# Kernel optimization log

Hardware: AMD Instinct MI355X
Metric: run time of the kernel (lower is better)

Reference implementation:

```python
import math
import jax, jax.numpy as jnp
import numpy as np

HIDDEN = 1024
INTER = 2048
NUM_EXPERTS = 8          # includes 1 noop slot (last column)
TOP_K = 2
CAPACITY_FACTOR = 1.0
BATCH, SEQ = 4, 4096


def setup_inputs() -> dict:
    key = jax.random.key(0)
    k_x, k_rw, k_ei, k_eo = jax.random.split(key, 4)
    x = jax.random.normal(k_x, (BATCH, SEQ, HIDDEN), dtype=jnp.float32)
    # Router: nn.Linear(hidden, num_experts) with xavier_uniform weight, zero-ish bias
    limit = math.sqrt(6.0 / (HIDDEN + NUM_EXPERTS))
    router_w = jax.random.uniform(k_rw, (NUM_EXPERTS, HIDDEN), dtype=jnp.float32,
                                  minval=-limit, maxval=limit)
    router_b = jnp.zeros((NUM_EXPERTS,), dtype=jnp.float32)
    # Expert params initialized with randn, exactly as in the torch module
    experts_inter = jax.random.normal(k_ei, (NUM_EXPERTS - 1, HIDDEN, INTER), dtype=jnp.float32)
    experts_out = jax.random.normal(k_eo, (NUM_EXPERTS - 1, INTER, HIDDEN), dtype=jnp.float32)
    return {"x": x, "router_w": router_w, "router_b": router_b,
            "experts_inter": experts_inter, "experts_out": experts_out}


def reference(x, router_w, router_b, experts_inter, experts_out):
    B, S, H = x.shape
    E = router_w.shape[0]
    N = B * S
    capacity = math.ceil(N / E * CAPACITY_FACTOR)  # static (shapes are static)

    x_flat = x.reshape(N, H)
    # Router: linear + softmax over experts
    weights = jax.nn.softmax(x_flat @ router_w.T + router_b, axis=-1)   # [N, E]

    # Top-k sparsification: keep top-k weights per token, zero the rest
    vals, idx = jax.lax.top_k(weights, TOP_K)                            # [N, k]
    topk_w = jnp.zeros_like(weights).at[jnp.arange(N)[:, None], idx].set(vals)

    # Last expert column is the no-op (identity) path
    noop_routed = x_flat * topk_w[:, -1:]                                # [N, H]

    expert_w = topk_w[:, :-1]                                            # [N, E-1]
    mask = (expert_w > 0).astype(jnp.int32)                              # [N, E-1]

    # Per-expert: sort tokens by routing mask (descending), take first `capacity`
    sorted_idx = jnp.argsort(-mask, axis=0)[:capacity]                   # [C, E-1], stable
    sorted_mask = jnp.take_along_axis(mask, sorted_idx, axis=0)          # [C, E-1]

    used_idx = (sorted_idx * sorted_mask).reshape(-1)                    # [C*(E-1)]
    toks = x_flat[used_idx] * sorted_mask.reshape(-1)[:, None].astype(x.dtype)
    toks = toks.reshape(capacity, E - 1, H)                              # [C, E-1, H]
    in_w = jnp.take_along_axis(expert_w, sorted_idx, axis=0)             # [C, E-1]

    # Grouped expert FFN: relu(x W1) W2, weighted by routing prob
    h = jax.nn.relu(jnp.einsum('ceh,ehi->cei', toks, experts_inter))     # [C, E-1, I]
    out = jnp.einsum('cei,eih->ceh', h, experts_out) * in_w[..., None]   # [C, E-1, H]

    # Scatter-add combine (masked slots contribute zeros at index 0)
    combined = jnp.zeros_like(x_flat).at[used_idx].add(out.reshape(-1, H))
    combined = combined + noop_routed
    return combined.reshape(B, S, H)
```

## Files before the change

### kernel.cpp

```cpp
#include <hip/hip_runtime.h>
#include <stdint.h>

#define HIDDEN 1024
#define INTER 2048
#define NEXP 8
#define NE 7
#define NTOK 16384
#define CAP 2048
#define BM 64
#define BN 64
#define BK 64
#define GBM 128
#define GBN 128

typedef __attribute__((ext_vector_type(8))) short short8;
typedef __attribute__((ext_vector_type(4))) float f32x4;

__device__ __forceinline__ unsigned short f2bf(float f) {
  union { float f; unsigned int u; } v;
  v.f = f;
  unsigned int u = v.u;
  unsigned int r = (u + 0x7FFFu + ((u >> 16) & 1u)) >> 16;
  return (unsigned short)r;
}

typedef __attribute__((address_space(1))) const unsigned int gu32;
typedef __attribute__((address_space(3))) unsigned int lu32;
__device__ __forceinline__ void gload16(const void* g, void* l) {
  __builtin_amdgcn_global_load_lds((gu32*)g, (lu32*)l, 16, 0, 0);
}

__global__ __launch_bounds__(256) void router_kernel(
    const float* __restrict__ x, const float* __restrict__ rw,
    const float* __restrict__ rb, float* __restrict__ expw,
    float* __restrict__ noopw) {
  int wid = threadIdx.x >> 6;
  int lane = threadIdx.x & 63;
  int token = blockIdx.x * 4 + wid;
  const float* xr = x + (size_t)token * HIDDEN;
  float acc[NEXP];
#pragma unroll
  for (int e = 0; e < NEXP; e++) acc[e] = 0.f;
#pragma unroll
  for (int j = 0; j < HIDDEN / 64; j++) {
    int k = j * 64 + lane;
    float xv = xr[k];
#pragma unroll
    for (int e = 0; e < NEXP; e++) acc[e] = fmaf(xv, rw[e * HIDDEN + k], acc[e]);
  }
#pragma unroll
  for (int e = 0; e < NEXP; e++) {
    float a = acc[e];
#pragma unroll
    for (int off = 32; off > 0; off >>= 1) a += __shfl_xor(a, off);
    acc[e] = a + rb[e];
  }
  if (lane == 0) {
    float m = acc[0];
#pragma unroll
    for (int e = 1; e < NEXP; e++) m = fmaxf(m, acc[e]);
    float w[NEXP];
    float s = 0.f;
#pragma unroll
    for (int e = 0; e < NEXP; e++) { w[e] = expf(acc[e] - m); s += w[e]; }
    float inv = 1.f / s;
#pragma unroll
    for (int e = 0; e < NEXP; e++) w[e] *= inv;
    int t1 = 0;
#pragma unroll
    for (int e = 1; e < NEXP; e++) if (w[e] > w[t1]) t1 = e;
    int t2 = (t1 == 0) ? 1 : 0;
#pragma unroll
    for (int e = 0; e < NEXP; e++) if (e != t1 && w[e] > w[t2]) t2 = e;
    noopw[token] = (t1 == NEXP - 1) ? w[t1] : ((t2 == NEXP - 1) ? w[t2] : 0.f);
#pragma unroll
    for (int e = 0; e < NE; e++) {
      float v = 0.f;
      if (e == t1) v = w[e];
      if (e == t2) v = w[e];
      expw[(size_t)e * NTOK + token] = v;
    }
  }
}

__global__ void assign_kernel(const float* __restrict__ expw,
                              int* __restrict__ slot_tok,
                              float* __restrict__ slot_w) {
  int e = blockIdx.x;
  int lane = threadIdx.x;
  const float* we = expw + (size_t)e * NTOK;
  int base = 0;
  for (int t0 = 0; t0 < NTOK; t0 += 64) {
    float w = we[t0 + lane];
    bool flag = w > 0.f;
    unsigned long long mask = __ballot(flag);
    int prefix = __popcll(mask & ((1ull << lane) - 1ull));
    int pos = base + prefix;
    if (flag && pos < CAP) {
      slot_tok[e * CAP + pos] = t0 + lane;
      slot_w[e * CAP + pos] = w;
    }
    base += __popcll(mask);
    if (base >= CAP) break;
  }
  int cnt = base < CAP ? base : CAP;
  for (int p = cnt + lane; p < CAP; p += 64) {
    slot_tok[e * CAP + p] = -1;
    slot_w[e * CAP + p] = 0.f;
  }
}

__global__ __launch_bounds__(256) void noop_kernel(
    const float* __restrict__ x, const float* __restrict__ noopw,
    float* __restrict__ out) {
  size_t i = (size_t)blockIdx.x * 256 + threadIdx.x;
  float4 v = ((const float4*)x)[i];
  float w = noopw[i >> 8];
  v.x *= w; v.y *= w; v.z *= w; v.w *= w;
  ((float4*)out)[i] = v;
}

__global__ __launch_bounds__(256) void convert_x_kernel(
    const float* __restrict__ x, unsigned short* __restrict__ xbf) {
  size_t i = (size_t)blockIdx.x * 256 + threadIdx.x;
  if (i >= (size_t)(NTOK + 1) * (HIDDEN / 8)) return;
  size_t row = i >> 7;
  short8 p;
  if (row < NTOK) {
    const float* s = x + i * 8;
    float4 v0 = ((const float4*)s)[0];
    float4 v1 = ((const float4*)s)[1];
    p[0] = (short)f2bf(v0.x); p[1] = (short)f2bf(v0.y);
    p[2] = (short)f2bf(v0.z); p[3] = (short)f2bf(v0.w);
    p[4] = (short)f2bf(v1.x); p[5] = (short)f2bf(v1.y);
    p[6] = (short)f2bf(v1.z); p[7] = (short)f2bf(v1.w);
  } else {
    p = (short8){0, 0, 0, 0, 0, 0, 0, 0};
  }
  *(short8*)(xbf + i * 8) = p;
}

__global__ __launch_bounds__(256) void transpose_bf16_kernel(
    const float* __restrict__ in, unsigned short* __restrict__ outp,
    int K, int N) {
  int e = blockIdx.z;
  const float* src = in + (size_t)e * K * N;
  unsigned short* dst = outp + (size_t)e * K * N;
  int k0 = blockIdx.y * 64;
  int n0 = blockIdx.x * 64;
  __shared__ float tile[64][65];
  int tid = threadIdx.x;
  int nr = tid & 15;
  int kr = tid >> 4;
#pragma unroll
  for (int i = 0; i < 4; i++) {
    int k = i * 16 + kr;
    float4 v = *(const float4*)(src + (size_t)(k0 + k) * N + n0 + nr * 4);
    tile[k][nr * 4 + 0] = v.x;
    tile[k][nr * 4 + 1] = v.y;
    tile[k][nr * 4 + 2] = v.z;
    tile[k][nr * 4 + 3] = v.w;
  }
  __syncthreads();
  int g = tid & 7;
  int nb = tid >> 3;
#pragma unroll
  for (int i = 0; i < 2; i++) {
    int n = i * 32 + nb;
    short8 p;
#pragma unroll
    for (int j = 0; j < 8; j++) p[j] = (short)f2bf(tile[g * 8 + j][n]);
    *(short8*)(dst + (size_t)(n0 + n) * K + k0 + g * 8) = p;
  }
}

__global__ __launch_bounds__(256) void gemm1_mfma_kernel(
    const unsigned short* __restrict__ xbf, const unsigned short* __restrict__ wiT,
    const int* __restrict__ slot_tok, unsigned short* __restrict__ h) {
  int e = blockIdx.z;
  const unsigned short* be = wiT + (size_t)e * HIDDEN * INTER;
  unsigned short* he = h + (size_t)e * CAP * INTER;
  int bm0 = blockIdx.y * GBM;
  int bn0 = blockIdx.x * GBN;
  __shared__ __align__(16) unsigned short As[GBM * 64];
  __shared__ __align__(16) unsigned short Bs[GBN * 64];
  int tid = threadIdx.x;
  int lane = tid & 63, w = tid >> 6;
  int wm = w >> 1, wn = w & 1;

  const unsigned short* aptr[4];
  const unsigned short* bptr[4];
#pragma unroll
  for (int c = 0; c < 4; c++) {
    int s = w * 4 + c;
    int r = s * 8 + (lane >> 3);
    int gb = lane & 7;
    int g = gb ^ (r & 7);
    int tok = slot_tok[e * CAP + bm0 + r];
    int row = tok < 0 ? NTOK : tok;
    aptr[c] = xbf + (size_t)row * HIDDEN + g * 8;
    bptr[c] = be + (size_t)(bn0 + r) * HIDDEN + g * 8;
  }

  f32x4 acc[4][4];
#pragma unroll
  for (int i = 0; i < 4; i++)
#pragma unroll
    for (int j = 0; j < 4; j++) acc[i][j] = (f32x4){0.f, 0.f, 0.f, 0.f};

  for (int k0 = 0; k0 < HIDDEN; k0 += 64) {
#pragma unroll
    for (int c = 0; c < 4; c++) gload16(aptr[c] + k0, &As[(w * 4 + c) * 512]);
#pragma unroll
    for (int c = 0; c < 4; c++) gload16(bptr[c] + k0, &Bs[(w * 4 + c) * 512]);
    __syncthreads();
#pragma unroll
    for (int kk = 0; kk < 2; kk++) {
      short8 a[4], b[4];
#pragma unroll
      for (int fm = 0; fm < 4; fm++) {
        int r = wm * 64 + fm * 16 + (lane & 15);
        int gb = (kk * 4 + (lane >> 4)) ^ (r & 7);
        a[fm] = *(const short8*)&As[r * 64 + gb * 8];
      }
#pragma unroll
      for (int fn = 0; fn < 4; fn++) {
        int n = wn * 64 + fn * 16 + (lane & 15);
        int gb = (kk * 4 + (lane >> 4)) ^ (n & 7);
        b[fn] = *(const short8*)&Bs[n * 64 + gb * 8];
      }
#pragma unroll
      for (int fm = 0; fm < 4; fm++)
#pragma unroll
        for (int fn = 0; fn < 4; fn++)
          acc[fm][fn] = __builtin_amdgcn_mfma_f32_16x16x32_bf16(
              a[fm], b[fn], acc[fm][fn], 0, 0, 0);
    }
    __syncthreads();
  }
#pragma unroll
  for (int fm = 0; fm < 4; fm++)
#pragma unroll
    for (int r4 = 0; r4 < 4; r4++) {
      int m = bm0 + wm * 64 + fm * 16 + ((lane >> 4) << 2) + r4;
#pragma unroll
      for (int fn = 0; fn < 4; fn++) {
        int n = bn0 + wn * 64 + fn * 16 + (lane & 15);
        float v = acc[fm][fn][r4];
        he[(size_t)m * INTER + n] = f2bf(v > 0.f ? v : 0.f);
      }
    }
}

__global__ __launch_bounds__(256) void gemm2_mfma_kernel(
    const unsigned short* __restrict__ h, const unsigned short* __restrict__ woT,
    const int* __restrict__ slot_tok, const float* __restrict__ slot_w,
    float* __restrict__ out) {
  int e = blockIdx.z;
  const unsigned short* ae = h + (size_t)e * CAP * INTER;
  const unsigned short* be = woT + (size_t)e * INTER * HIDDEN;
  int bm0 = blockIdx.y * GBM;
  int bn0 = blockIdx.x * GBN;
  __shared__ __align__(16) unsigned short As[GBM * 64];
  __shared__ __align__(16) unsigned short Bs[GBN * 64];
  int tid = threadIdx.x;
  int lane = tid & 63, w = tid >> 6;
  int wm = w >> 1, wn = w & 1;

  const unsigned short* aptr[4];
  const unsigned short* bptr[4];
#pragma unroll
  for (int c = 0; c < 4; c++) {
    int s = w * 4 + c;
    int r = s * 8 + (lane >> 3);
    int gb = lane & 7;
    int g = gb ^ (r & 7);
    aptr[c] = ae + (size_t)(bm0 + r) * INTER + g * 8;
    bptr[c] = be + (size_t)(bn0 + r) * INTER + g * 8;
  }

  f32x4 acc[4][4];
#pragma unroll
  for (int i = 0; i < 4; i++)
#pragma unroll
    for (int j = 0; j < 4; j++) acc[i][j] = (f32x4){0.f, 0.f, 0.f, 0.f};

  for (int k0 = 0; k0 < INTER; k0 += 64) {
#pragma unroll
    for (int c = 0; c < 4; c++) gload16(aptr[c] + k0, &As[(w * 4 + c) * 512]);
#pragma unroll
    for (int c = 0; c < 4; c++) gload16(bptr[c] + k0, &Bs[(w * 4 + c) * 512]);
    __syncthreads();
#pragma unroll
    for (int kk = 0; kk < 2; kk++) {
      short8 a[4], b[4];
#pragma unroll
      for (int fm = 0; fm < 4; fm++) {
        int r = wm * 64 + fm * 16 + (lane & 15);
        int gb = (kk * 4 + (lane >> 4)) ^ (r & 7);
        a[fm] = *(const short8*)&As[r * 64 + gb * 8];
      }
#pragma unroll
      for (int fn = 0; fn < 4; fn++) {
        int n = wn * 64 + fn * 16 + (lane & 15);
        int gb = (kk * 4 + (lane >> 4)) ^ (n & 7);
        b[fn] = *(const short8*)&Bs[n * 64 + gb * 8];
      }
#pragma unroll
      for (int fm = 0; fm < 4; fm++)
#pragma unroll
        for (int fn = 0; fn < 4; fn++)
          acc[fm][fn] = __builtin_amdgcn_mfma_f32_16x16x32_bf16(
              a[fm], b[fn], acc[fm][fn], 0, 0, 0);
    }
    __syncthreads();
  }
#pragma unroll
  for (int fm = 0; fm < 4; fm++)
#pragma unroll
    for (int r4 = 0; r4 < 4; r4++) {
      int m = bm0 + wm * 64 + fm * 16 + ((lane >> 4) << 2) + r4;
      int tok = slot_tok[e * CAP + m];
      float sw = slot_w[e * CAP + m];
      if (tok >= 0) {
#pragma unroll
        for (int fn = 0; fn < 4; fn++) {
          int n = bn0 + wn * 64 + fn * 16 + (lane & 15);
          unsafeAtomicAdd(out + (size_t)tok * HIDDEN + n, acc[fm][fn][r4] * sw);
        }
      }
    }
}

__global__ __launch_bounds__(256) void gemm1_kernel(
    const float* __restrict__ x, const float* __restrict__ wi,
    const int* __restrict__ slot_tok, unsigned short* __restrict__ h,
    int e_base) {
  int e = e_base + blockIdx.z;
  unsigned short* he = h + (size_t)blockIdx.z * ((size_t)CAP * INTER);
  const float* wie = wi + (size_t)e * HIDDEN * INTER;
  int bm0 = blockIdx.y * BM;
  int bn0 = blockIdx.x * BN;
  __shared__ __align__(16) unsigned short As[BM][BK];
  __shared__ __align__(16) unsigned short Bs[BN][BK];
  int tid = threadIdx.x;
  int lane = tid & 63;
  int wid = tid >> 6;
  int wm = wid >> 1, wn = wid & 1;
  int tokA[2];
#pragma unroll
  for (int t = 0; t < 2; t++)
    tokA[t] = slot_tok[e * CAP + bm0 + ((tid + t * 256) >> 3)];
  f32x4 acc[2][2];
#pragma unroll
  for (int i = 0; i < 2; i++)
#pragma unroll
    for (int j = 0; j < 2; j++) acc[i][j] = (f32x4){0.f, 0.f, 0.f, 0.f};
  for (int k0 = 0; k0 < HIDDEN; k0 += BK) {
#pragma unroll
    for (int t = 0; t < 2; t++) {
      int idx = tid + t * 256;
      int r = idx >> 3, g = idx & 7;
      short8 pack;
      if (tokA[t] >= 0) {
        const float* src = x + (size_t)tokA[t] * HIDDEN + k0 + g * 8;
        float4 v0 = ((const float4*)src)[0];
        float4 v1 = ((const float4*)src)[1];
        pack[0] = (short)f2bf(v0.x); pack[1] = (short)f2bf(v0.y);
        pack[2] = (short)f2bf(v0.z); pack[3] = (short)f2bf(v0.w);
        pack[4] = (short)f2bf(v1.x); pack[5] = (short)f2bf(v1.y);
        pack[6] = (short)f2bf(v1.z); pack[7] = (short)f2bf(v1.w);
      } else {
        pack = (short8){0, 0, 0, 0, 0, 0, 0, 0};
      }
      int gs = g ^ (r & 7);
      *(short8*)(&As[r][gs * 8]) = pack;
    }
#pragma unroll
    for (int t = 0; t < 2; t++) {
      int idx = tid + t * 256;
      int k = idx >> 3, g = idx & 7;
      const float* src = wie + (size_t)(k0 + k) * INTER + bn0 + g * 8;
      float4 v0 = ((const float4*)src)[0];
      float4 v1 = ((const float4*)src)[1];
      float f[8] = {v0.x, v0.y, v0.z, v0.w, v1.x, v1.y, v1.z, v1.w};
#pragma unroll
      for (int i2 = 0; i2 < 8; i2++) {
        int n = g * 8 + i2;
        int kc = k ^ ((n & 7) << 3);
        Bs[n][kc] = f2bf(f[i2]);
      }
    }
    __syncthreads();
#pragma unroll
    for (int kk = 0; kk < 2; kk++) {
      short8 a[2], b[2];
#pragma unroll
      for (int fm = 0; fm < 2; fm++) {
        int r = wm * 32 + fm * 16 + (lane & 15);
        int gs = (kk * 4 + (lane >> 4)) ^ (r & 7);
        a[fm] = *(const short8*)(&As[r][gs * 8]);
      }
#pragma unroll
      for (int fn = 0; fn < 2; fn++) {
        int n = wn * 32 + fn * 16 + (lane & 15);
        int gs = (kk * 4 + (lane >> 4)) ^ (n & 7);
        b[fn] = *(const short8*)(&Bs[n][gs * 8]);
      }
#pragma unroll
      for (int fm = 0; fm < 2; fm++)
#pragma unroll
        for (int fn = 0; fn < 2; fn++)
          acc[fm][fn] = __builtin_amdgcn_mfma_f32_16x16x32_bf16(
              a[fm], b[fn], acc[fm][fn], 0, 0, 0);
    }
    __syncthreads();
  }
#pragma unroll
  for (int fm = 0; fm < 2; fm++)
#pragma unroll
    for (int fn = 0; fn < 2; fn++)
#pragma unroll
      for (int r = 0; r < 4; r++) {
        int m = bm0 + wm * 32 + fm * 16 + ((lane >> 4) << 2) + r;
        int n = bn0 + wn * 32 + fn * 16 + (lane & 15);
        float v = acc[fm][fn][r];
        v = v > 0.f ? v : 0.f;
        he[(size_t)m * INTER + n] = f2bf(v);
      }
}

__global__ __launch_bounds__(256) void gemm2_kernel(
    const unsigned short* __restrict__ h, const float* __restrict__ wo,
    const int* __restrict__ slot_tok, const float* __restrict__ slot_w,
    float* __restrict__ out, int e_base) {
  int e = e_base + blockIdx.z;
  const unsigned short* he = h + (size_t)blockIdx.z * ((size_t)CAP * INTER);
  const float* woe = wo + (size_t)e * INTER * HIDDEN;
  int bm0 = blockIdx.y * BM;
  int bn0 = blockIdx.x * BN;
  __shared__ __align__(16) unsigned short As[BM][BK];
  __shared__ __align__(16) unsigned short Bs[BN][BK];
  int tid = threadIdx.x;
  int lane = tid & 63;
  int wid = tid >> 6;
  int wm = wid >> 1, wn = wid & 1;
  f32x4 acc[2][2];
#pragma unroll
  for (int i = 0; i < 2; i++)
#pragma unroll
    for (int j = 0; j < 2; j++) acc[i][j] = (f32x4){0.f, 0.f, 0.f, 0.f};
  for (int k0 = 0; k0 < INTER; k0 += BK) {
#pragma unroll
    for (int t = 0; t < 2; t++) {
      int idx = tid + t * 256;
      int r = idx >> 3, g = idx & 7;
      short8 pack = *(const short8*)(he + (size_t)(bm0 + r) * INTER + k0 + g * 8);
      int gs = g ^ (r & 7);
      *(short8*)(&As[r][gs * 8]) = pack;
    }
#pragma unroll
    for (int t = 0; t < 2; t++) {
      int idx = tid + t * 256;
      int k = idx >> 3, g = idx & 7;
      const float* src = woe + (size_t)(k0 + k) * HIDDEN + bn0 + g * 8;
      float4 v0 = ((const float4*)src)[0];
      float4 v1 = ((const float4*)src)[1];
      float f[8] = {v0.x, v0.y, v0.z, v0.w, v1.x, v1.y, v1.z, v1.w};
#pragma unroll
      for (int i2 = 0; i2 < 8; i2++) {
        int n = g * 8 + i2;
        int kc = k ^ ((n & 7) << 3);
        Bs[n][kc] = f2bf(f[i2]);
      }
    }
    __syncthreads();
#pragma unroll
    for (int kk = 0; kk < 2; kk++) {
      short8 a[2], b[2];
#pragma unroll
      for (int fm = 0; fm < 2; fm++) {
        int r = wm * 32 + fm * 16 + (lane & 15);
        int gs = (kk * 4 + (lane >> 4)) ^ (r & 7);
        a[fm] = *(const short8*)(&As[r][gs * 8]);
      }
#pragma unroll
      for (int fn = 0; fn < 2; fn++) {
        int n = wn * 32 + fn * 16 + (lane & 15);
        int gs = (kk * 4 + (lane >> 4)) ^ (n & 7);
        b[fn] = *(const short8*)(&Bs[n][gs * 8]);
      }
#pragma unroll
      for (int fm = 0; fm < 2; fm++)
#pragma unroll
        for (int fn = 0; fn < 2; fn++)
          acc[fm][fn] = __builtin_amdgcn_mfma_f32_16x16x32_bf16(
              a[fm], b[fn], acc[fm][fn], 0, 0, 0);
    }
    __syncthreads();
  }
#pragma unroll
  for (int fm = 0; fm < 2; fm++)
#pragma unroll
    for (int r = 0; r < 4; r++) {
      int m = bm0 + wm * 32 + fm * 16 + ((lane >> 4) << 2) + r;
      int tok = slot_tok[e * CAP + m];
      float sw = slot_w[e * CAP + m];
      if (tok >= 0) {
#pragma unroll
        for (int fn = 0; fn < 2; fn++) {
          int n = bn0 + wn * 32 + fn * 16 + (lane & 15);
          unsafeAtomicAdd(out + (size_t)tok * HIDDEN + n, acc[fm][fn][r] * sw);
        }
      }
    }
}

extern "C" void kernel_launch(void* const* d_in, const int* in_sizes, int n_in,
                              void* d_out, int out_size, void* d_ws, size_t ws_size,
                              hipStream_t stream) {
  const float* x = (const float*)d_in[0];
  const float* rw = (const float*)d_in[1];
  const float* rb = (const float*)d_in[2];
  const float* wi = (const float*)d_in[3];
  const float* wo = (const float*)d_in[4];
  float* out = (float*)d_out;
  char* ws = (char*)d_ws;

  const size_t h_bytes = (size_t)NE * CAP * INTER * 2;
  const size_t xbf_bytes = (size_t)(NTOK + 1) * HIDDEN * 2;
  const size_t wT_bytes = (size_t)NE * HIDDEN * INTER * 2;
  const size_t P_bytes = xbf_bytes + wT_bytes;
  const size_t small_bytes = (size_t)NE * NTOK * 4 + (size_t)NTOK * 4 +
                             (size_t)NE * CAP * 4 * 2;
  const size_t need_new = h_bytes + P_bytes + small_bytes;

  if (ws_size >= need_new) {
    unsigned short* h = (unsigned short*)ws;
    char* P = ws + h_bytes;
    unsigned short* xbf = (unsigned short*)P;
    unsigned short* wiT = (unsigned short*)(P + xbf_bytes);
    unsigned short* woT = (unsigned short*)P;
    char* smalls = P + P_bytes;
    float* expw = (float*)smalls;
    float* noopw = expw + (size_t)NE * NTOK;
    int* slot_tok = (int*)(noopw + NTOK);
    float* slot_w = (float*)(slot_tok + (size_t)NE * CAP);

    convert_x_kernel<<<((NTOK + 1) * (HIDDEN / 8) + 255) / 256, 256, 0, stream>>>(x, xbf);
    transpose_bf16_kernel<<<dim3(INTER / 64, HIDDEN / 64, NE), 256, 0, stream>>>(
        wi, wiT, HIDDEN, INTER);
    router_kernel<<<NTOK / 4, 256, 0, stream>>>(x, rw, rb, expw, noopw);
    assign_kernel<<<NE, 64, 0, stream>>>(expw, slot_tok, slot_w);
    noop_kernel<<<(NTOK * (HIDDEN / 4)) / 256, 256, 0, stream>>>(x, noopw, out);
    gemm1_mfma_kernel<<<dim3(INTER / GBN, CAP / GBM, NE), 256, 0, stream>>>(
        xbf, wiT, slot_tok, h);
    transpose_bf16_kernel<<<dim3(HIDDEN / 64, INTER / 64, NE), 256, 0, stream>>>(
        wo, woT, INTER, HIDDEN);
    gemm2_mfma_kernel<<<dim3(HIDDEN / GBN, CAP / GBM, NE), 256, 0, stream>>>(
        h, woT, slot_tok, slot_w, out);
    return;
  }

  const size_t h_full = (size_t)NE * CAP * INTER * 2;
  const size_t h_one = (size_t)CAP * INTER * 2;
  bool full = ws_size >= h_full + small_bytes;
  size_t hb = full ? h_full : h_one;
  unsigned short* h = (unsigned short*)ws;
  float* expw = (float*)(ws + hb);
  float* noopw = expw + (size_t)NE * NTOK;
  int* slot_tok = (int*)(noopw + NTOK);
  float* slot_w = (float*)(slot_tok + (size_t)NE * CAP);

  router_kernel<<<NTOK / 4, 256, 0, stream>>>(x, rw, rb, expw, noopw);
  assign_kernel<<<NE, 64, 0, stream>>>(expw, slot_tok, slot_w);
  noop_kernel<<<(NTOK * (HIDDEN / 4)) / 256, 256, 0, stream>>>(x, noopw, out);
  if (full) {
    gemm1_kernel<<<dim3(INTER / BN, CAP / BM, NE), 256, 0, stream>>>(
        x, wi, slot_tok, h, 0);
    gemm2_kernel<<<dim3(HIDDEN / BN, CAP / BM, NE), 256, 0, stream>>>(
        h, wo, slot_tok, slot_w, out, 0);
  } else {
    for (int e = 0; e < NE; e++) {
      gemm1_kernel<<<dim3(INTER / BN, CAP / BM, 1), 256, 0, stream>>>(
          x, wi, slot_tok, h, e);
      gemm2_kernel<<<dim3(HIDDEN / BN, CAP / BM, 1), 256, 0, stream>>>(
          h, wo, slot_tok, slot_w, out, e);
    }
  }
}
```

Baseline: 487.4 us.

## Fuse router, bf16 convert and noop into one prologue; parallelize assignment; swizzle GEMM blocks

```diff
diff --git a/kernel.cpp b/kernel.cpp
--- a/kernel.cpp
+++ b/kernel.cpp
@@ -28,6 +28,326 @@
 typedef __attribute__((address_space(3))) unsigned int lu32;
 __device__ __forceinline__ void gload16(const void* g, void* l) {
   __builtin_amdgcn_global_load_lds((gu32*)g, (lu32*)l, 16, 0, 0);
+}
+
+__global__ __launch_bounds__(256) void prologue_kernel(
+    const float* __restrict__ x, const float* __restrict__ rw,
+    const float* __restrict__ rb, float* __restrict__ expw,
+    float* __restrict__ noopw, unsigned short* __restrict__ xbf,
+    float* __restrict__ out) {
+  if (blockIdx.x == NTOK / 4) {
+    unsigned int* z = (unsigned int*)(xbf + (size_t)NTOK * HIDDEN);
+    z[threadIdx.x] = 0u;
+    z[threadIdx.x + 256] = 0u;
+    return;
+  }
+  int wid = threadIdx.x >> 6;
+  int lane = threadIdx.x & 63;
+  int token = blockIdx.x * 4 + wid;
+  const float* xr = x + (size_t)token * HIDDEN;
+  float4 xv[4];
+  float acc[NEXP];
+#pragma unroll
+  for (int e = 0; e < NEXP; e++) acc[e] = 0.f;
+#pragma unroll
+  for (int j = 0; j < 4; j++) {
+    xv[j] = *(const float4*)(xr + j * 256 + lane * 4);
+#pragma unroll
+    for (int e = 0; e < NEXP; e++) {
+      float4 wv = *(const float4*)(rw + e * HIDDEN + j * 256 + lane * 4);
+      acc[e] = fmaf(xv[j].x, wv.x, acc[e]);
+      acc[e] = fmaf(xv[j].y, wv.y, acc[e]);
+      acc[e] = fmaf(xv[j].z, wv.z, acc[e]);
+      acc[e] = fmaf(xv[j].w, wv.w, acc[e]);
+    }
+  }
+#pragma unroll
+  for (int e = 0; e < NEXP; e++) {
+    float a = acc[e];
+#pragma unroll
+    for (int off = 32; off > 0; off >>= 1) a += __shfl_xor(a, off);
+    acc[e] = a + rb[e];
+  }
+  float nwv = 0.f;
+  if (lane == 0) {
+    float m = acc[0];
+#pragma unroll
+    for (int e = 1; e < NEXP; e++) m = fmaxf(m, acc[e]);
+    float w[NEXP];
+    float s = 0.f;
+#pragma unroll
+    for (int e = 0; e < NEXP; e++) { w[e] = expf(acc[e] - m); s += w[e]; }
+    float inv = 1.f / s;
+#pragma unroll
+    for (int e = 0; e < NEXP; e++) w[e] *= inv;
+    int t1 = 0;
+#pragma unroll
+    for (int e = 1; e < NEXP; e++) if (w[e] > w[t1]) t1 = e;
+    int t2 = (t1 == 0) ? 1 : 0;
+#pragma unroll
+    for (int e = 0; e < NEXP; e++) if (e != t1 && w[e] > w[t2]) t2 = e;
+    nwv = (t1 == NEXP - 1) ? w[t1] : ((t2 == NEXP - 1) ? w[t2] : 0.f);
+    noopw[token] = nwv;
+#pragma unroll
+    for (int e = 0; e < NE; e++) {
+      float v = 0.f;
+      if (e == t1) v = w[e];
+      if (e == t2) v = w[e];
+      expw[(size_t)e * NTOK + token] = v;
+    }
+  }
+  float nw = __shfl(nwv, 0);
+  float* orow = out + (size_t)token * HIDDEN;
+  unsigned short* brow = xbf + (size_t)token * HIDDEN;
+#pragma unroll
+  for (int j = 0; j < 4; j++) {
+    float4 o = xv[j];
+    o.x *= nw; o.y *= nw; o.z *= nw; o.w *= nw;
+    *(float4*)(orow + j * 256 + lane * 4) = o;
+    ushort4 b;
+    b.x = f2bf(xv[j].x); b.y = f2bf(xv[j].y);
+    b.z = f2bf(xv[j].z); b.w = f2bf(xv[j].w);
+    *(ushort4*)(brow + j * 256 + lane * 4) = b;
+  }
+}
+
+__global__ __launch_bounds__(1024) void assign_par_kernel(
+    const float* __restrict__ expw, int* __restrict__ slot_tok,
+    float* __restrict__ slot_w) {
+  int e = blockIdx.x;
+  int tid = threadIdx.x;
+  int lane = tid & 63, w = tid >> 6;
+  __shared__ int wtot[16];
+  const float* we = expw + (size_t)e * NTOK;
+  int base = 0;
+#pragma unroll 1
+  for (int r = 0; r < NTOK / 1024; r++) {
+    int t = r * 1024 + tid;
+    float wv = we[t];
+    bool flag = wv > 0.f;
+    unsigned long long mask = __ballot(flag);
+    int lp = __popcll(mask & ((1ull << lane) - 1ull));
+    if (lane == 0) wtot[w] = __popcll(mask);
+    __syncthreads();
+    int pre = 0, tot = 0;
+#pragma unroll
+    for (int i = 0; i < 16; i++) {
+      int v = wtot[i];
+      pre += (i < w) ? v : 0;
+      tot += v;
+    }
+    int pos = base + pre + lp;
+    if (flag && pos < CAP) {
+      slot_tok[e * CAP + pos] = t;
+      slot_w[e * CAP + pos] = wv;
+    }
+    base += tot;
+    __syncthreads();
+    if (base >= CAP) break;
+  }
+  int cnt = base < CAP ? base : CAP;
+  for (int p = cnt + tid; p < CAP; p += 1024) {
+    slot_tok[e * CAP + p] = -1;
+    slot_w[e * CAP + p] = 0.f;
+  }
+}
+
+__global__ __launch_bounds__(256) void transpose_bf16_kernel(
+    const float* __restrict__ in, unsigned short* __restrict__ outp,
+    int K, int N) {
+  int e = blockIdx.z;
+  const float* src = in + (size_t)e * K * N;
+  unsigned short* dst = outp + (size_t)e * K * N;
+  int k0 = blockIdx.y * 64;
+  int n0 = blockIdx.x * 64;
+  __shared__ float tile[64][65];
+  int tid = threadIdx.x;
+  int nr = tid & 15;
+  int kr = tid >> 4;
+#pragma unroll
+  for (int i = 0; i < 4; i++) {
+    int k = i * 16 + kr;
+    float4 v = *(const float4*)(src + (size_t)(k0 + k) * N + n0 + nr * 4);
+    tile[k][nr * 4 + 0] = v.x;
+    tile[k][nr * 4 + 1] = v.y;
+    tile[k][nr * 4 + 2] = v.z;
+    tile[k][nr * 4 + 3] = v.w;
+  }
+  __syncthreads();
+  int g = tid & 7;
+  int nb = tid >> 3;
+#pragma unroll
+  for (int i = 0; i < 2; i++) {
+    int n = i * 32 + nb;
+    short8 p;
+#pragma unroll
+    for (int j = 0; j < 8; j++) p[j] = (short)f2bf(tile[g * 8 + j][n]);
+    *(short8*)(dst + (size_t)(n0 + n) * K + k0 + g * 8) = p;
+  }
+}
+
+__global__ __launch_bounds__(256) void gemm1_mfma_kernel(
+    const unsigned short* __restrict__ xbf, const unsigned short* __restrict__ wiT,
+    const int* __restrict__ slot_tok, unsigned short* __restrict__ h) {
+  int orig = blockIdx.x + (blockIdx.y << 4) + (blockIdx.z << 8);
+  int swz = (orig & 7) * 224 + (orig >> 3);
+  int bxi = swz & 15, byi = (swz >> 4) & 15, bzi = swz >> 8;
+  int e = bzi;
+  const unsigned short* be = wiT + (size_t)e * HIDDEN * INTER;
+  unsigned short* he = h + (size_t)e * CAP * INTER;
+  int bm0 = byi * GBM;
+  int bn0 = bxi * GBN;
+  __shared__ __align__(16) unsigned short As[GBM * 64];
+  __shared__ __align__(16) unsigned short Bs[GBN * 64];
+  int tid = threadIdx.x;
+  int lane = tid & 63, w = tid >> 6;
+  int wm = w >> 1, wn = w & 1;
+
+  const unsigned short* aptr[4];
+  const unsigned short* bptr[4];
+#pragma unroll
+  for (int c = 0; c < 4; c++) {
+    int s = w * 4 + c;
+    int r = s * 8 + (lane >> 3);
+    int gb = lane & 7;
+    int g = gb ^ (r & 7);
+    int tok = slot_tok[e * CAP + bm0 + r];
+    int row = tok < 0 ? NTOK : tok;
+    aptr[c] = xbf + (size_t)row * HIDDEN + g * 8;
+    bptr[c] = be + (size_t)(bn0 + r) * HIDDEN + g * 8;
+  }
+
+  f32x4 acc[4][4];
+#pragma unroll
+  for (int i = 0; i < 4; i++)
+#pragma unroll
+    for (int j = 0; j < 4; j++) acc[i][j] = (f32x4){0.f, 0.f, 0.f, 0.f};
+
+  for (int k0 = 0; k0 < HIDDEN; k0 += 64) {
+#pragma unroll
+    for (int c = 0; c < 4; c++) gload16(aptr[c] + k0, &As[(w * 4 + c) * 512]);
+#pragma unroll
+    for (int c = 0; c < 4; c++) gload16(bptr[c] + k0, &Bs[(w * 4 + c) * 512]);
+    __syncthreads();
+#pragma unroll
+    for (int kk = 0; kk < 2; kk++) {
+      short8 a[4], b[4];
+#pragma unroll
+      for (int fm = 0; fm < 4; fm++) {
+        int r = wm * 64 + fm * 16 + (lane & 15);
+        int gb = (kk * 4 + (lane >> 4)) ^ (r & 7);
+        a[fm] = *(const short8*)&As[r * 64 + gb * 8];
+      }
+#pragma unroll
+      for (int fn = 0; fn < 4; fn++) {
+        int n = wn * 64 + fn * 16 + (lane & 15);
+        int gb = (kk * 4 + (lane >> 4)) ^ (n & 7);
+        b[fn] = *(const short8*)&Bs[n * 64 + gb * 8];
+      }
+#pragma unroll
+      for (int fm = 0; fm < 4; fm++)
+#pragma unroll
+        for (int fn = 0; fn < 4; fn++)
+          acc[fm][fn] = __builtin_amdgcn_mfma_f32_16x16x32_bf16(
+              a[fm], b[fn], acc[fm][fn], 0, 0, 0);
+    }
+    __syncthreads();
+  }
+#pragma unroll
+  for (int fm = 0; fm < 4; fm++)
+#pragma unroll
+    for (int r4 = 0; r4 < 4; r4++) {
+      int m = bm0 + wm * 64 + fm * 16 + ((lane >> 4) << 2) + r4;
+#pragma unroll
+      for (int fn = 0; fn < 4; fn++) {
+        int n = bn0 + wn * 64 + fn * 16 + (lane & 15);
+        float v = acc[fm][fn][r4];
+        he[(size_t)m * INTER + n] = f2bf(v > 0.f ? v : 0.f);
+      }
+    }
+}
+
+__global__ __launch_bounds__(256) void gemm2_mfma_kernel(
+    const unsigned short* __restrict__ h, const unsigned short* __restrict__ woT,
+    const int* __restrict__ slot_tok, const float* __restrict__ slot_w,
+    float* __restrict__ out) {
+  int orig = blockIdx.x + (blockIdx.y << 3) + (blockIdx.z << 7);
+  int swz = (orig & 7) * 112 + (orig >> 3);
+  int bxi = swz & 7, byi = (swz >> 3) & 15, bzi = swz >> 7;
+  int e = bzi;
+  const unsigned short* ae = h + (size_t)e * CAP * INTER;
+  const unsigned short* be = woT + (size_t)e * INTER * HIDDEN;
+  int bm0 = byi * GBM;
+  int bn0 = bxi * GBN;
+  __shared__ __align__(16) unsigned short As[GBM * 64];
+  __shared__ __align__(16) unsigned short Bs[GBN * 64];
+  int tid = threadIdx.x;
+  int lane = tid & 63, w = tid >> 6;
+  int wm = w >> 1, wn = w & 1;
+
+  const unsigned short* aptr[4];
+  const unsigned short* bptr[4];
+#pragma unroll
+  for (int c = 0; c < 4; c++) {
+    int s = w * 4 + c;
+    int r = s * 8 + (lane >> 3);
+    int gb = lane & 7;
+    int g = gb ^ (r & 7);
+    aptr[c] = ae + (size_t)(bm0 + r) * INTER + g * 8;
+    bptr[c] = be + (size_t)(bn0 + r) * INTER + g * 8;
+  }
+
+  f32x4 acc[4][4];
+#pragma unroll
+  for (int i = 0; i < 4; i++)
+#pragma unroll
+    for (int j = 0; j < 4; j++) acc[i][j] = (f32x4){0.f, 0.f, 0.f, 0.f};
+
+  for (int k0 = 0; k0 < INTER; k0 += 64) {
+#pragma unroll
+    for (int c = 0; c < 4; c++) gload16(aptr[c] + k0, &As[(w * 4 + c) * 512]);
+#pragma unroll
+    for (int c = 0; c < 4; c++) gload16(bptr[c] + k0, &Bs[(w * 4 + c) * 512]);
+    __syncthreads();
+#pragma unroll
+    for (int kk = 0; kk < 2; kk++) {
+      short8 a[4], b[4];
+#pragma unroll
+      for (int fm = 0; fm < 4; fm++) {
+        int r = wm * 64 + fm * 16 + (lane & 15);
+        int gb = (kk * 4 + (lane >> 4)) ^ (r & 7);
+        a[fm] = *(const short8*)&As[r * 64 + gb * 8];
+      }
+#pragma unroll
+      for (int fn = 0; fn < 4; fn++) {
+        int n = wn * 64 + fn * 16 + (lane & 15);
+        int gb = (kk * 4 + (lane >> 4)) ^ (n & 7);
+        b[fn] = *(const short8*)&Bs[n * 64 + gb * 8];
+      }
+#pragma unroll
+      for (int fm = 0; fm < 4; fm++)
+#pragma unroll
+        for (int fn = 0; fn < 4; fn++)
+          acc[fm][fn] = __builtin_amdgcn_mfma_f32_16x16x32_bf16(
+              a[fm], b[fn], acc[fm][fn], 0, 0, 0);
+    }
+    __syncthreads();
+  }
+#pragma unroll
+  for (int fm = 0; fm < 4; fm++)
+#pragma unroll
+    for (int r4 = 0; r4 < 4; r4++) {
+      int m = bm0 + wm * 64 + fm * 16 + ((lane >> 4) << 2) + r4;
+      int tok = slot_tok[e * CAP + m];
+      float sw = slot_w[e * CAP + m];
+      if (tok >= 0) {
+#pragma unroll
+        for (int fn = 0; fn < 4; fn++) {
+          int n = bn0 + wn * 64 + fn * 16 + (lane & 15);
+          unsafeAtomicAdd(out + (size_t)tok * HIDDEN + n, acc[fm][fn][r4] * sw);
+        }
+      }
+    }
 }
 
 __global__ __launch_bounds__(256) void router_kernel(
@@ -120,218 +440,6 @@
   ((float4*)out)[i] = v;
 }
 
-__global__ __launch_bounds__(256) void convert_x_kernel(
-    const float* __restrict__ x, unsigned short* __restrict__ xbf) {
-  size_t i = (size_t)blockIdx.x * 256 + threadIdx.x;
-  if (i >= (size_t)(NTOK + 1) * (HIDDEN / 8)) return;
-  size_t row = i >> 7;
-  short8 p;
-  if (row < NTOK) {
-    const float* s = x + i * 8;
-    float4 v0 = ((const float4*)s)[0];
-    float4 v1 = ((const float4*)s)[1];
-    p[0] = (short)f2bf(v0.x); p[1] = (short)f2bf(v0.y);
-    p[2] = (short)f2bf(v0.z); p[3] = (short)f2bf(v0.w);
-    p[4] = (short)f2bf(v1.x); p[5] = (short)f2bf(v1.y);
-    p[6] = (short)f2bf(v1.z); p[7] = (short)f2bf(v1.w);
-  } else {
-    p = (short8){0, 0, 0, 0, 0, 0, 0, 0};
-  }
-  *(short8*)(xbf + i * 8) = p;
-}
-
-__global__ __launch_bounds__(256) void transpose_bf16_kernel(
-    const float* __restrict__ in, unsigned short* __restrict__ outp,
-    int K, int N) {
-  int e = blockIdx.z;
-  const float* src = in + (size_t)e * K * N;
-  unsigned short* dst = outp + (size_t)e * K * N;
-  int k0 = blockIdx.y * 64;
-  int n0 = blockIdx.x * 64;
-  __shared__ float tile[64][65];
-  int tid = threadIdx.x;
-  int nr = tid & 15;
-  int kr = tid >> 4;
-#pragma unroll
-  for (int i = 0; i < 4; i++) {
-    int k = i * 16 + kr;
-    float4 v = *(const float4*)(src + (size_t)(k0 + k) * N + n0 + nr * 4);
-    tile[k][nr * 4 + 0] = v.x;
-    tile[k][nr * 4 + 1] = v.y;
-    tile[k][nr * 4 + 2] = v.z;
-    tile[k][nr * 4 + 3] = v.w;
-  }
-  __syncthreads();
-  int g = tid & 7;
-  int nb = tid >> 3;
-#pragma unroll
-  for (int i = 0; i < 2; i++) {
-    int n = i * 32 + nb;
-    short8 p;
-#pragma unroll
-    for (int j = 0; j < 8; j++) p[j] = (short)f2bf(tile[g * 8 + j][n]);
-    *(short8*)(dst + (size_t)(n0 + n) * K + k0 + g * 8) = p;
-  }
-}
-
-__global__ __launch_bounds__(256) void gemm1_mfma_kernel(
-    const unsigned short* __restrict__ xbf, const unsigned short* __restrict__ wiT,
-    const int* __restrict__ slot_tok, unsigned short* __restrict__ h) {
-  int e = blockIdx.z;
-  const unsigned short* be = wiT + (size_t)e * HIDDEN * INTER;
-  unsigned short* he = h + (size_t)e * CAP * INTER;
-  int bm0 = blockIdx.y * GBM;
-  int bn0 = blockIdx.x * GBN;
-  __shared__ __align__(16) unsigned short As[GBM * 64];
-  __shared__ __align__(16) unsigned short Bs[GBN * 64];
-  int tid = threadIdx.x;
-  int lane = tid & 63, w = tid >> 6;
-  int wm = w >> 1, wn = w & 1;
-
-  const unsigned short* aptr[4];
-  const unsigned short* bptr[4];
-#pragma unroll
-  for (int c = 0; c < 4; c++) {
-    int s = w * 4 + c;
-    int r = s * 8 + (lane >> 3);
-    int gb = lane & 7;
-    int g = gb ^ (r & 7);
-    int tok = slot_tok[e * CAP + bm0 + r];
-    int row = tok < 0 ? NTOK : tok;
-    aptr[c] = xbf + (size_t)row * HIDDEN + g * 8;
-    bptr[c] = be + (size_t)(bn0 + r) * HIDDEN + g * 8;
-  }
-
-  f32x4 acc[4][4];
-#pragma unroll
-  for (int i = 0; i < 4; i++)
-#pragma unroll
-    for (int j = 0; j < 4; j++) acc[i][j] = (f32x4){0.f, 0.f, 0.f, 0.f};
-
-  for (int k0 = 0; k0 < HIDDEN; k0 += 64) {
-#pragma unroll
-    for (int c = 0; c < 4; c++) gload16(aptr[c] + k0, &As[(w * 4 + c) * 512]);
-#pragma unroll
-    for (int c = 0; c < 4; c++) gload16(bptr[c] + k0, &Bs[(w * 4 + c) * 512]);
-    __syncthreads();
-#pragma unroll
-    for (int kk = 0; kk < 2; kk++) {
-      short8 a[4], b[4];
-#pragma unroll
-      for (int fm = 0; fm < 4; fm++) {
-        int r = wm * 64 + fm * 16 + (lane & 15);
-        int gb = (kk * 4 + (lane >> 4)) ^ (r & 7);
-        a[fm] = *(const short8*)&As[r * 64 + gb * 8];
-      }
-#pragma unroll
-      for (int fn = 0; fn < 4; fn++) {
-        int n = wn * 64 + fn * 16 + (lane & 15);
-        int gb = (kk * 4 + (lane >> 4)) ^ (n & 7);
-        b[fn] = *(const short8*)&Bs[n * 64 + gb * 8];
-      }
-#pragma unroll
-      for (int fm = 0; fm < 4; fm++)
-#pragma unroll
-        for (int fn = 0; fn < 4; fn++)
-          acc[fm][fn] = __builtin_amdgcn_mfma_f32_16x16x32_bf16(
-              a[fm], b[fn], acc[fm][fn], 0, 0, 0);
-    }
-    __syncthreads();
-  }
-#pragma unroll
-  for (int fm = 0; fm < 4; fm++)
-#pragma unroll
-    for (int r4 = 0; r4 < 4; r4++) {
-      int m = bm0 + wm * 64 + fm * 16 + ((lane >> 4) << 2) + r4;
-#pragma unroll
-      for (int fn = 0; fn < 4; fn++) {
-        int n = bn0 + wn * 64 + fn * 16 + (lane & 15);
-        float v = acc[fm][fn][r4];
-        he[(size_t)m * INTER + n] = f2bf(v > 0.f ? v : 0.f);
-      }
-    }
-}
-
-__global__ __launch_bounds__(256) void gemm2_mfma_kernel(
-    const unsigned short* __restrict__ h, const unsigned short* __restrict__ woT,
-    const int* __restrict__ slot_tok, const float* __restrict__ slot_w,
-    float* __restrict__ out) {
-  int e = blockIdx.z;
-  const unsigned short* ae = h + (size_t)e * CAP * INTER;
-  const unsigned short* be = woT + (size_t)e * INTER * HIDDEN;
-  int bm0 = blockIdx.y * GBM;
-  int bn0 = blockIdx.x * GBN;
-  __shared__ __align__(16) unsigned short As[GBM * 64];
-  __shared__ __align__(16) unsigned short Bs[GBN * 64];
-  int tid = threadIdx.x;
-  int lane = tid & 63, w = tid >> 6;
-  int wm = w >> 1, wn = w & 1;
-
-  const unsigned short* aptr[4];
-  const unsigned short* bptr[4];
-#pragma unroll
-  for (int c = 0; c < 4; c++) {
-    int s = w * 4 + c;
-    int r = s * 8 + (lane >> 3);
-    int gb = lane & 7;
-    int g = gb ^ (r & 7);
-    aptr[c] = ae + (size_t)(bm0 + r) * INTER + g * 8;
-    bptr[c] = be + (size_t)(bn0 + r) * INTER + g * 8;
-  }
-
-  f32x4 acc[4][4];
-#pragma unroll
-  for (int i = 0; i < 4; i++)
-#pragma unroll
-    for (int j = 0; j < 4; j++) acc[i][j] = (f32x4){0.f, 0.f, 0.f, 0.f};
-
-  for (int k0 = 0; k0 < INTER; k0 += 64) {
-#pragma unroll
-    for (int c = 0; c < 4; c++) gload16(aptr[c] + k0, &As[(w * 4 + c) * 512]);
-#pragma unroll
-    for (int c = 0; c < 4; c++) gload16(bptr[c] + k0, &Bs[(w * 4 + c) * 512]);
-    __syncthreads();
-#pragma unroll
-    for (int kk = 0; kk < 2; kk++) {
-      short8 a[4], b[4];
-#pragma unroll
-      for (int fm = 0; fm < 4; fm++) {
-        int r = wm * 64 + fm * 16 + (lane & 15);
-        int gb = (kk * 4 + (lane >> 4)) ^ (r & 7);
-        a[fm] = *(const short8*)&As[r * 64 + gb * 8];
-      }
-#pragma unroll
-      for (int fn = 0; fn < 4; fn++) {
-        int n = wn * 64 + fn * 16 + (lane & 15);
-        int gb = (kk * 4 + (lane >> 4)) ^ (n & 7);
-        b[fn] = *(const short8*)&Bs[n * 64 + gb * 8];
-      }
-#pragma unroll
-      for (int fm = 0; fm < 4; fm++)
-#pragma unroll
-        for (int fn = 0; fn < 4; fn++)
-          acc[fm][fn] = __builtin_amdgcn_mfma_f32_16x16x32_bf16(
-              a[fm], b[fn], acc[fm][fn], 0, 0, 0);
-    }
-    __syncthreads();
-  }
-#pragma unroll
-  for (int fm = 0; fm < 4; fm++)
-#pragma unroll
-    for (int r4 = 0; r4 < 4; r4++) {
-      int m = bm0 + wm * 64 + fm * 16 + ((lane >> 4) << 2) + r4;
-      int tok = slot_tok[e * CAP + m];
-      float sw = slot_w[e * CAP + m];
-      if (tok >= 0) {
-#pragma unroll
-        for (int fn = 0; fn < 4; fn++) {
-          int n = bn0 + wn * 64 + fn * 16 + (lane & 15);
-          unsafeAtomicAdd(out + (size_t)tok * HIDDEN + n, acc[fm][fn][r4] * sw);
-        }
-      }
-    }
-}
-
 __global__ __launch_bounds__(256) void gemm1_kernel(
     const float* __restrict__ x, const float* __restrict__ wi,
     const int* __restrict__ slot_tok, unsigned short* __restrict__ h,
@@ -547,12 +655,11 @@
     int* slot_tok = (int*)(noopw + NTOK);
     float* slot_w = (float*)(slot_tok + (size_t)NE * CAP);
 
-    convert_x_kernel<<<((NTOK + 1) * (HIDDEN / 8) + 255) / 256, 256, 0, stream>>>(x, xbf);
+    prologue_kernel<<<NTOK / 4 + 1, 256, 0, stream>>>(x, rw, rb, expw, noopw,
+                                                      xbf, out);
+    assign_par_kernel<<<NE, 1024, 0, stream>>>(expw, slot_tok, slot_w);
     transpose_bf16_kernel<<<dim3(INTER / 64, HIDDEN / 64, NE), 256, 0, stream>>>(
         wi, wiT, HIDDEN, INTER);
-    router_kernel<<<NTOK / 4, 256, 0, stream>>>(x, rw, rb, expw, noopw);
-    assign_kernel<<<NE, 64, 0, stream>>>(expw, slot_tok, slot_w);
-    noop_kernel<<<(NTOK * (HIDDEN / 4)) / 256, 256, 0, stream>>>(x, noopw, out);
     gemm1_mfma_kernel<<<dim3(INTER / GBN, CAP / GBM, NE), 256, 0, stream>>>(
         xbf, wiT, slot_tok, h);
     transpose_bf16_kernel<<<dim3(HIDDEN / 64, INTER / 64, NE), 256, 0, stream>>>(
```

Result: faster. 430.3 us (-11.7%).
